# Performance work log

Hardware: AMD Instinct MI355X
Metric: run time of the kernel (lower is better)

The kernel has to match this reference:

```python
import jax, jax.numpy as jnp
import numpy as np

K_HOPS = 10  # truncation order of the heat-kernel Taylor series


def setup_inputs() -> dict:
    key = jax.random.key(0)
    k1, k2, k3 = jax.random.split(key, 3)
    N, E, D_IN, D_OUT = 50000, 625000, 128, 128
    x = jax.random.normal(k1, (N, D_IN), dtype=jnp.float32)
    edge_index = jax.random.randint(k2, (2, E), 0, N, dtype=jnp.int64)
    t = jnp.asarray(5.0, dtype=jnp.float32)  # learnable diffusion time
    lim = 1.0 / np.sqrt(D_IN)
    W = jax.random.uniform(k3, (D_OUT, D_IN), dtype=jnp.float32, minval=-lim, maxval=lim)
    b = jnp.zeros((D_OUT,), dtype=jnp.float32)
    return {"x": x, "edge_index": edge_index, "t": t, "W": W, "b": b}


def reference(x, edge_index, t, W, b):
    N = x.shape[0]
    loop = jnp.arange(N, dtype=edge_index.dtype)
    src = jnp.concatenate([edge_index[0], loop])  # gcn_norm adds self-loops
    dst = jnp.concatenate([edge_index[1], loop])
    # symmetric normalization: norm_e = deg(dst)^-1/2 * deg(src)^-1/2
    deg = jnp.zeros((N,), dtype=x.dtype).at[dst].add(1.0)
    dinv = jnp.where(deg > 0, jax.lax.rsqrt(deg), 0.0)
    norm = dinv[src] * dinv[dst]  # [E+N]

    def prop(h):  # one hop of A_hat @ h via gather-scale-scatter
        msg = h[src] * norm[:, None]          # [E+N, D]
        return jax.ops.segment_sum(msg, dst, num_segments=N)

    # heat kernel: e^{-t} * sum_k t^k/k! * A_hat^k x
    coeff = jnp.exp(-t)
    out = coeff * x
    h = x
    for k in range(1, K_HOPS + 1):
        h = prop(h)
        coeff = coeff * t / k
        out = out + coeff * h
    return out @ W.T + b
```

## Files before the change

kernel.cpp:

```cpp
#include <hip/hip_runtime.h>
#include <math.h>

typedef float f4 __attribute__((ext_vector_type(4)));
typedef float f8 __attribute__((ext_vector_type(8)));
typedef _Float16 h8 __attribute__((ext_vector_type(8)));
typedef int i4 __attribute__((ext_vector_type(4)));


__global__ void k_count(const int* __restrict__ dst, int* __restrict__ cnt, int E) {
  int e = blockIdx.x * blockDim.x + threadIdx.x;
  if (e < E) atomicAdd(&cnt[dst[e]], 1);
}

__global__ void k_scan_partial(const int* __restrict__ cnt, int* __restrict__ rowptr,
                               int* __restrict__ bsums, float* __restrict__ dinv,
                               float* __restrict__ rdinv, int N) {
  __shared__ int s[1024];
  int tid = threadIdx.x;
  int idx = blockIdx.x * 1024 + tid;
  int v = (idx < N) ? cnt[idx] : 0;
  if (idx < N) {
    dinv[idx] = rsqrtf((float)(v + 1));
    rdinv[idx] = sqrtf((float)(v + 1));
  }
  int vp = (v + 3) & ~3;
  s[tid] = vp;
  __syncthreads();
  for (int off = 1; off < 1024; off <<= 1) {
    int add = (tid >= off) ? s[tid - off] : 0;
    __syncthreads();
    s[tid] += add;
    __syncthreads();
  }
  if (idx <= N) rowptr[idx] = s[tid] - vp;
  if (tid == 1023) bsums[blockIdx.x] = s[1023];
}

__global__ void k_scan_sums(int* __restrict__ bsums, int nb) {
  __shared__ int s[1024];
  int tid = threadIdx.x;
  int v = (tid < nb) ? bsums[tid] : 0;
  s[tid] = v;
  __syncthreads();
  for (int off = 1; off < 1024; off <<= 1) {
    int add = (tid >= off) ? s[tid - off] : 0;
    __syncthreads();
    s[tid] += add;
    __syncthreads();
  }
  if (tid < nb) bsums[tid] = s[tid] - v;
}

__global__ void k_add_offsets(int* __restrict__ rowptr, int* __restrict__ cursor,
                              const int* __restrict__ bsums, int N) {
  int idx = blockIdx.x * 1024 + threadIdx.x;
  if (idx <= N) {
    int v = rowptr[idx] + bsums[blockIdx.x];
    rowptr[idx] = v;
    if (idx < N) cursor[idx] = v;
  }
}

__global__ void k_scatter(const int* __restrict__ src, const int* __restrict__ dst,
                          int* __restrict__ cursor, int* __restrict__ col, int E) {
  int e = blockIdx.x * blockDim.x + threadIdx.x;
  if (e < E) {
    int d = dst[e];
    int slot = atomicAdd(&cursor[d], 1);
    col[slot] = src[e];
  }
}

__global__ void k_padfill(const int* __restrict__ rowptr, const int* __restrict__ cursor,
                          int* __restrict__ col, int N) {
  int r = blockIdx.x * blockDim.x + threadIdx.x;
  if (r < N) {
    int e = cursor[r], end = rowptr[r + 1];
    for (; e < end; ++e) col[e] = N;
  }
}

__global__ void k_tohalf(const float* __restrict__ x, _Float16* __restrict__ xz,
                         const float* __restrict__ dinv, _Float16* __restrict__ z0,
                         _Float16* __restrict__ z1, int total8) {
  int i = blockIdx.x * blockDim.x + threadIdx.x;
  if (i < total8) {
    float d = dinv[i >> 4];
    f4 a = ((const f4*)x)[i * 2], b = ((const f4*)x)[i * 2 + 1];
    f8 v = {a.x, a.y, a.z, a.w, b.x, b.y, b.z, b.w};
    ((h8*)xz)[i] = __builtin_convertvector(d * v, h8);
  } else if (i < total8 + 48) {
    int k = i - total8;
    h8 zero = {0, 0, 0, 0, 0, 0, 0, 0};
    if (k < 16) ((h8*)xz)[total8 + k] = zero;
    else if (k < 32) ((h8*)z0)[total8 + (k - 16)] = zero;
    else ((h8*)z1)[total8 + (k - 32)] = zero;
  }
}

__global__ __launch_bounds__(256) void k_hop(
    const int* __restrict__ rowptr, const int* __restrict__ col,
    const float* __restrict__ dinv, const h8* __restrict__ xz,
    const h8* __restrict__ zin, h8* __restrict__ zout,
    const float* __restrict__ t_ptr, int j, int first, int N) {
  int wave = threadIdx.x >> 6;
  int lane = threadIdx.x & 63;
  int grp = lane >> 3;
  int r = (blockIdx.x * 4 + wave) * 4 + (grp >> 1);
  if (r >= N) return;
  int fl = (lane & 7) + (grp & 1) * 8;
  float t = t_ptr[0];
  float cj = expf(-t);
  for (int i = 1; i <= j; ++i) cj *= t / (float)i;
  float gs = first ? cj * t / (float)(j + 1) : 1.0f;

  auto G = [&](int idx) -> f8 {
    return __builtin_convertvector(zin[(size_t)idx * 16 + fl], f8);
  };

  f8 sA = {0, 0, 0, 0, 0, 0, 0, 0}, sB = sA, sC = sA, sD = sA;
  int e = rowptr[r], end = rowptr[r + 1];
  int cnt = end - e;
  const i4* q = (const i4*)&col[e];
  int it8 = cnt >> 3;
  int tail4 = cnt & 7;

  i4 p0 = {0, 0, 0, 0}, p1 = p0;
  if (it8) {
    p0 = q[0]; p1 = q[1];
    q += 2;
  }
  for (int i = 1; i < it8; ++i) {
    i4 n0 = q[0], n1 = q[1];
    q += 2;
    sA += G(p0.x);
    sB += G(p0.y);
    sC += G(p0.z);
    sD += G(p0.w);
    sA += G(p1.x);
    sB += G(p1.y);
    sC += G(p1.z);
    sD += G(p1.w);
    p0 = n0; p1 = n1;
  }
  if (it8) {
    sA += G(p0.x);
    sB += G(p0.y);
    sC += G(p0.z);
    sD += G(p0.w);
    sA += G(p1.x);
    sB += G(p1.y);
    sC += G(p1.z);
    sD += G(p1.w);
  }
  if (tail4) {
    i4 a0 = q[0];
    sA += G(a0.x);
    sB += G(a0.y);
    sC += G(a0.z);
    sD += G(a0.w);
  }

  f8 s = (sA + sB) + (sC + sD);
  s += G(r);
  float di = dinv[r];
  float sc = gs * di * di;
  f8 xr = __builtin_convertvector(xz[(size_t)r * 16 + fl], f8);
  s = sc * s + cj * xr;
  zout[(size_t)r * 16 + fl] = __builtin_convertvector(s, h8);
}

__global__ __launch_bounds__(256) void k_matmul(
    const h8* __restrict__ z16, const float* __restrict__ W,
    const float* __restrict__ bias, const float* __restrict__ rdinv,
    float* __restrict__ out, int N) {
  __shared__ h8 whiS[128 * 16];
  __shared__ h8 wloS[128 * 16];
  int tid = threadIdx.x;
  int rblk = blockIdx.x * 128;

#pragma unroll
  for (int it = 0; it < 8; ++it) {
    int idx = it * 256 + tid;
    int n = idx >> 4, g = idx & 15;
    f4 a = *(const f4*)&W[(size_t)n * 128 + g * 8];
    f4 b = *(const f4*)&W[(size_t)n * 128 + g * 8 + 4];
    f8 w = {a.x, a.y, a.z, a.w, b.x, b.y, b.z, b.w};
    h8 hi = __builtin_convertvector(w, h8);
    f8 hir = __builtin_convertvector(hi, f8);
    h8 lo = __builtin_convertvector(w - hir, h8);
    int slot = n * 16 + (g ^ (n & 7));
    whiS[slot] = hi;
    wloS[slot] = lo;
  }
  __syncthreads();

  int wave = tid >> 6, lane = tid & 63;
  int q = lane >> 4, fl = lane & 15;
  int rbase = rblk + wave * 32;

  f4 acc[2][8];
#pragma unroll
  for (int rt = 0; rt < 2; ++rt)
#pragma unroll
    for (int nt = 0; nt < 8; ++nt) acc[rt][nt] = (f4){0.f, 0.f, 0.f, 0.f};

#pragma unroll
  for (int s = 0; s < 4; ++s) {
    h8 aA, aB;
    {
      int r0 = rbase + fl;       if (r0 >= N) r0 = N - 1;
      int r1 = rbase + 16 + fl;  if (r1 >= N) r1 = N - 1;
      aA = z16[(size_t)r0 * 16 + s * 4 + q];
      aB = z16[(size_t)r1 * 16 + s * 4 + q];
    }
#pragma unroll
    for (int nt = 0; nt < 8; ++nt) {
      int n = nt * 16 + fl;
      int slot = n * 16 + ((s * 4 + q) ^ (n & 7));
      h8 bh = whiS[slot];
      h8 bl = wloS[slot];
      acc[0][nt] = __builtin_amdgcn_mfma_f32_16x16x32_f16(aA, bh, acc[0][nt], 0, 0, 0);
      acc[0][nt] = __builtin_amdgcn_mfma_f32_16x16x32_f16(aA, bl, acc[0][nt], 0, 0, 0);
      acc[1][nt] = __builtin_amdgcn_mfma_f32_16x16x32_f16(aB, bh, acc[1][nt], 0, 0, 0);
      acc[1][nt] = __builtin_amdgcn_mfma_f32_16x16x32_f16(aB, bl, acc[1][nt], 0, 0, 0);
    }
  }

#pragma unroll
  for (int rt = 0; rt < 2; ++rt) {
#pragma unroll
    for (int reg = 0; reg < 4; ++reg) {
      int r = rbase + rt * 16 + q * 4 + reg;
      if (r < N) {
        float rd = rdinv[r];
#pragma unroll
        for (int nt = 0; nt < 8; ++nt) {
          out[(size_t)r * 128 + nt * 16 + fl] =
              acc[rt][nt][reg] * rd + bias[nt * 16 + fl];
        }
      }
    }
  }
}


extern "C" void kernel_launch(void* const* d_in, const int* in_sizes, int n_in,
                              void* d_out, int out_size, void* d_ws, size_t ws_size,
                              hipStream_t stream) {
  const float* x = (const float*)d_in[0];
  const int* ei = (const int*)d_in[1];
  const float* t = (const float*)d_in[2];
  const float* W = (const float*)d_in[3];
  const float* b = (const float*)d_in[4];
  int N = in_sizes[0] / 128;
  int E = in_sizes[1] / 2;
  const int* srcp = ei;
  const int* dstp = ei + E;
  float* out = (float*)d_out;

  char* ws = (char*)d_ws;
  size_t off = 0;
  auto alloc = [&](size_t bytes) -> void* {
    void* p = ws + off;
    off += (bytes + 255) & ~(size_t)255;
    return p;
  };
  h8*    zh0    = (h8*)alloc((size_t)(N + 1) * 128 * 2);
  h8*    zh1    = (h8*)alloc((size_t)(N + 1) * 128 * 2);
  h8*    xz     = (h8*)alloc((size_t)(N + 1) * 128 * 2);
  int*   cnt    = (int*)alloc((size_t)N * 4);
  float* dinv   = (float*)alloc((size_t)N * 4);
  float* rdinv  = (float*)alloc((size_t)N * 4);
  int*   rowptr = (int*)alloc((size_t)(N + 1) * 4);
  int*   cursor = (int*)alloc((size_t)N * 4);
  int*   bsums  = (int*)alloc(4096);
  size_t col_bytes = ((size_t)E + 4 * (size_t)N) * 4;
  int*   col    = (int*)alloc(col_bytes);
  (void)ws_size;

  int nb_scan = (N + 1 + 1023) / 1024;

  hipMemsetAsync(cnt, 0, (size_t)N * 4, stream);
  k_count<<<(E + 255) / 256, 256, 0, stream>>>(dstp, cnt, E);
  k_scan_partial<<<nb_scan, 1024, 0, stream>>>(cnt, rowptr, bsums, dinv, rdinv, N);
  k_scan_sums<<<1, 1024, 0, stream>>>(bsums, nb_scan);
  k_add_offsets<<<nb_scan, 1024, 0, stream>>>(rowptr, cursor, bsums, N);
  k_scatter<<<(E + 255) / 256, 256, 0, stream>>>(srcp, dstp, cursor, col, E);
  k_padfill<<<(N + 255) / 256, 256, 0, stream>>>(rowptr, cursor, col, N);
  k_tohalf<<<(N * 16 + 48 + 255) / 256, 256, 0, stream>>>(x, (_Float16*)xz, dinv,
                                                          (_Float16*)zh0, (_Float16*)zh1,
                                                          N * 16);

  int nblk = (N + 15) / 16;
  const h8* zin = xz;
  h8* bufs[2] = {zh0, zh1};
  for (int m = 0; m < 10; ++m) {
    h8* zout = bufs[m & 1];
    k_hop<<<nblk, 256, 0, stream>>>(rowptr, col, dinv, xz, zin, zout,
                                    t, 9 - m, (m == 0) ? 1 : 0, N);
    zin = zout;
  }

  k_matmul<<<(N + 127) / 128, 256, 0, stream>>>(zin, W, b, rdinv, out, N);
}
```

Baseline: 430.4 us.

## Bucket CSR neighbours by source range to improve gather locality

Builds the CSR adjacency with four sub-rows per destination node, each holding neighbours from one quarter of the source index range. The hop kernel walks the four sub-rows in order so that concurrently running waves gather from a narrower range of feature rows, aiming for better cache hit rates. In exchange, each sub-row is padded to a multiple of four, which adds dummy gathers. The scan, count and row-pointer arrays also grow fourfold, and the hop loop loses its deeper 8-wide prefetch unroll.

```diff
diff --git a/kernel.cpp b/kernel.cpp
--- a/kernel.cpp
+++ b/kernel.cpp
@@ -7,9 +7,14 @@
 typedef int i4 __attribute__((ext_vector_type(4)));
 
 
-__global__ void k_count(const int* __restrict__ dst, int* __restrict__ cnt, int E) {
+__global__ void k_count(const int* __restrict__ src, const int* __restrict__ dst,
+                        int* __restrict__ cnt, float invb, int E) {
   int e = blockIdx.x * blockDim.x + threadIdx.x;
-  if (e < E) atomicAdd(&cnt[dst[e]], 1);
+  if (e < E) {
+    int b = (int)((float)src[e] * invb);
+    b = b > 3 ? 3 : b;
+    atomicAdd(&cnt[dst[e] * 4 + b], 1);
+  }
 }
 
 __global__ void k_scan_partial(const int* __restrict__ cnt, int* __restrict__ rowptr,
@@ -18,10 +23,12 @@
   __shared__ int s[1024];
   int tid = threadIdx.x;
   int idx = blockIdx.x * 1024 + tid;
-  int v = (idx < N) ? cnt[idx] : 0;
+  int M = 4 * N;
+  int v = (idx < M) ? cnt[idx] : 0;
   if (idx < N) {
-    dinv[idx] = rsqrtf((float)(v + 1));
-    rdinv[idx] = sqrtf((float)(v + 1));
+    int deg = cnt[4 * idx] + cnt[4 * idx + 1] + cnt[4 * idx + 2] + cnt[4 * idx + 3];
+    dinv[idx] = rsqrtf((float)(deg + 1));
+    rdinv[idx] = sqrtf((float)(deg + 1));
   }
   int vp = (v + 3) & ~3;
   s[tid] = vp;
@@ -32,7 +39,7 @@
     s[tid] += add;
     __syncthreads();
   }
-  if (idx <= N) rowptr[idx] = s[tid] - vp;
+  if (idx <= M) rowptr[idx] = s[tid] - vp;
   if (tid == 1023) bsums[blockIdx.x] = s[1023];
 }
 
@@ -54,28 +61,32 @@
 __global__ void k_add_offsets(int* __restrict__ rowptr, int* __restrict__ cursor,
                               const int* __restrict__ bsums, int N) {
   int idx = blockIdx.x * 1024 + threadIdx.x;
-  if (idx <= N) {
+  int M = 4 * N;
+  if (idx <= M) {
     int v = rowptr[idx] + bsums[blockIdx.x];
     rowptr[idx] = v;
-    if (idx < N) cursor[idx] = v;
+    if (idx < M) cursor[idx] = v;
   }
 }
 
 __global__ void k_scatter(const int* __restrict__ src, const int* __restrict__ dst,
-                          int* __restrict__ cursor, int* __restrict__ col, int E) {
+                          int* __restrict__ cursor, int* __restrict__ col,
+                          float invb, int E) {
   int e = blockIdx.x * blockDim.x + threadIdx.x;
   if (e < E) {
-    int d = dst[e];
-    int slot = atomicAdd(&cursor[d], 1);
-    col[slot] = src[e];
+    int s = src[e];
+    int b = (int)((float)s * invb);
+    b = b > 3 ? 3 : b;
+    int slot = atomicAdd(&cursor[dst[e] * 4 + b], 1);
+    col[slot] = s;
   }
 }
 
 __global__ void k_padfill(const int* __restrict__ rowptr, const int* __restrict__ cursor,
                           int* __restrict__ col, int N) {
-  int r = blockIdx.x * blockDim.x + threadIdx.x;
-  if (r < N) {
-    int e = cursor[r], end = rowptr[r + 1];
+  int idx = blockIdx.x * blockDim.x + threadIdx.x;
+  if (idx < 4 * N) {
+    int e = cursor[idx], end = rowptr[idx + 1];
     for (; e < end; ++e) col[e] = N;
   }
 }
@@ -119,46 +130,27 @@
   };
 
   f8 sA = {0, 0, 0, 0, 0, 0, 0, 0}, sB = sA, sC = sA, sD = sA;
-  int e = rowptr[r], end = rowptr[r + 1];
-  int cnt = end - e;
-  const i4* q = (const i4*)&col[e];
-  int it8 = cnt >> 3;
-  int tail4 = cnt & 7;
-
-  i4 p0 = {0, 0, 0, 0}, p1 = p0;
-  if (it8) {
-    p0 = q[0]; p1 = q[1];
-    q += 2;
-  }
-  for (int i = 1; i < it8; ++i) {
-    i4 n0 = q[0], n1 = q[1];
-    q += 2;
-    sA += G(p0.x);
-    sB += G(p0.y);
-    sC += G(p0.z);
-    sD += G(p0.w);
-    sA += G(p1.x);
-    sB += G(p1.y);
-    sC += G(p1.z);
-    sD += G(p1.w);
-    p0 = n0; p1 = n1;
-  }
-  if (it8) {
-    sA += G(p0.x);
-    sB += G(p0.y);
-    sC += G(p0.z);
-    sD += G(p0.w);
-    sA += G(p1.x);
-    sB += G(p1.y);
-    sC += G(p1.z);
-    sD += G(p1.w);
-  }
-  if (tail4) {
-    i4 a0 = q[0];
-    sA += G(a0.x);
-    sB += G(a0.y);
-    sC += G(a0.z);
-    sD += G(a0.w);
+  int base = r * 4;
+#pragma unroll
+  for (int b = 0; b < 4; ++b) {
+    int e = rowptr[base + b], end = rowptr[base + b + 1];
+    const i4* q = (const i4*)&col[e];
+    int n4 = (end - e) >> 2;
+    if (n4) {
+      i4 p = q[0];
+      for (int i = 1; i < n4; ++i) {
+        i4 nx = q[i];
+        sA += G(p.x);
+        sB += G(p.y);
+        sC += G(p.z);
+        sD += G(p.w);
+        p = nx;
+      }
+      sA += G(p.x);
+      sB += G(p.y);
+      sC += G(p.z);
+      sD += G(p.w);
+    }
   }
 
   f8 s = (sA + sB) + (sC + sD);
@@ -269,25 +261,28 @@
   h8*    zh0    = (h8*)alloc((size_t)(N + 1) * 128 * 2);
   h8*    zh1    = (h8*)alloc((size_t)(N + 1) * 128 * 2);
   h8*    xz     = (h8*)alloc((size_t)(N + 1) * 128 * 2);
-  int*   cnt    = (int*)alloc((size_t)N * 4);
+  int*   cnt    = (int*)alloc((size_t)N * 16);
   float* dinv   = (float*)alloc((size_t)N * 4);
   float* rdinv  = (float*)alloc((size_t)N * 4);
-  int*   rowptr = (int*)alloc((size_t)(N + 1) * 4);
-  int*   cursor = (int*)alloc((size_t)N * 4);
+  int*   rowptr = (int*)alloc((size_t)(4 * N + 1) * 4);
+  int*   cursor = (int*)alloc((size_t)N * 16);
   int*   bsums  = (int*)alloc(4096);
-  size_t col_bytes = ((size_t)E + 4 * (size_t)N) * 4;
+  size_t col_bytes = ((size_t)E + 16 * (size_t)N) * 4;
   int*   col    = (int*)alloc(col_bytes);
   (void)ws_size;
 
-  int nb_scan = (N + 1 + 1023) / 1024;
-
-  hipMemsetAsync(cnt, 0, (size_t)N * 4, stream);
-  k_count<<<(E + 255) / 256, 256, 0, stream>>>(dstp, cnt, E);
+  int bsize = (N + 3) >> 2;
+  float invb = 1.0f / (float)bsize;
+
+  int nb_scan = (4 * N + 1 + 1023) / 1024;
+
+  hipMemsetAsync(cnt, 0, (size_t)N * 16, stream);
+  k_count<<<(E + 255) / 256, 256, 0, stream>>>(srcp, dstp, cnt, invb, E);
   k_scan_partial<<<nb_scan, 1024, 0, stream>>>(cnt, rowptr, bsums, dinv, rdinv, N);
   k_scan_sums<<<1, 1024, 0, stream>>>(bsums, nb_scan);
   k_add_offsets<<<nb_scan, 1024, 0, stream>>>(rowptr, cursor, bsums, N);
-  k_scatter<<<(E + 255) / 256, 256, 0, stream>>>(srcp, dstp, cursor, col, E);
-  k_padfill<<<(N + 255) / 256, 256, 0, stream>>>(rowptr, cursor, col, N);
+  k_scatter<<<(E + 255) / 256, 256, 0, stream>>>(srcp, dstp, cursor, col, invb, E);
+  k_padfill<<<(4 * N + 255) / 256, 256, 0, stream>>>(rowptr, cursor, col, N);
   k_tohalf<<<(N * 16 + 48 + 255) / 256, 256, 0, stream>>>(x, (_Float16*)xz, dinv,
                                                           (_Float16*)zh0, (_Float16*)zh1,
                                                           N * 16);
```

Result: slower. 444.3 us (+3.2%).

## Split feature dimension into two half-planes and run hops per half

Applied to the files above, without the earlier changes.

Stores the fp16 features as two 64-column planes instead of 128-column rows, and runs the ten diffusion hops separately on each plane, with one row per 8-lane group. The aim is to halve the gathered working set per hop so that the random neighbour gathers hit in cache more often. In exchange the CSR index array is read twice and twice as many hop kernels are launched. The matmul reads its A operand from the two planes.

```diff
diff --git a/kernel.cpp b/kernel.cpp
--- a/kernel.cpp
+++ b/kernel.cpp
@@ -82,40 +82,43 @@
 
 __global__ void k_tohalf(const float* __restrict__ x, _Float16* __restrict__ xz,
                          const float* __restrict__ dinv, _Float16* __restrict__ z0,
-                         _Float16* __restrict__ z1, int total8) {
+                         _Float16* __restrict__ z1, int total8, int N) {
   int i = blockIdx.x * blockDim.x + threadIdx.x;
+  size_t plane = (size_t)(N + 1) * 8;
   if (i < total8) {
-    float d = dinv[i >> 4];
+    int row = i >> 4, g = i & 15;
+    float d = dinv[row];
     f4 a = ((const f4*)x)[i * 2], b = ((const f4*)x)[i * 2 + 1];
     f8 v = {a.x, a.y, a.z, a.w, b.x, b.y, b.z, b.w};
-    ((h8*)xz)[i] = __builtin_convertvector(d * v, h8);
+    ((h8*)xz)[(size_t)(g >> 3) * plane + (size_t)row * 8 + (g & 7)] =
+        __builtin_convertvector(d * v, h8);
   } else if (i < total8 + 48) {
     int k = i - total8;
     h8 zero = {0, 0, 0, 0, 0, 0, 0, 0};
-    if (k < 16) ((h8*)xz)[total8 + k] = zero;
-    else if (k < 32) ((h8*)z0)[total8 + (k - 16)] = zero;
-    else ((h8*)z1)[total8 + (k - 32)] = zero;
+    int buf = k >> 4, sl = k & 15;
+    h8* base = buf == 0 ? (h8*)xz : (buf == 1 ? (h8*)z0 : (h8*)z1);
+    base[(size_t)(sl >> 3) * plane + (size_t)N * 8 + (sl & 7)] = zero;
   }
 }
 
 __global__ __launch_bounds__(256) void k_hop(
     const int* __restrict__ rowptr, const int* __restrict__ col,
-    const float* __restrict__ dinv, const h8* __restrict__ xz,
-    const h8* __restrict__ zin, h8* __restrict__ zout,
+    const float* __restrict__ dinv, const h8* __restrict__ xzp,
+    const h8* __restrict__ zinp, h8* __restrict__ zoutp,
     const float* __restrict__ t_ptr, int j, int first, int N) {
   int wave = threadIdx.x >> 6;
   int lane = threadIdx.x & 63;
   int grp = lane >> 3;
-  int r = (blockIdx.x * 4 + wave) * 4 + (grp >> 1);
+  int r = (blockIdx.x * 4 + wave) * 8 + grp;
   if (r >= N) return;
-  int fl = (lane & 7) + (grp & 1) * 8;
+  int fl = lane & 7;
   float t = t_ptr[0];
   float cj = expf(-t);
   for (int i = 1; i <= j; ++i) cj *= t / (float)i;
   float gs = first ? cj * t / (float)(j + 1) : 1.0f;
 
   auto G = [&](int idx) -> f8 {
-    return __builtin_convertvector(zin[(size_t)idx * 16 + fl], f8);
+    return __builtin_convertvector(zinp[(size_t)idx * 8 + fl], f8);
   };
 
   f8 sA = {0, 0, 0, 0, 0, 0, 0, 0}, sB = sA, sC = sA, sD = sA;
@@ -165,9 +168,9 @@
   s += G(r);
   float di = dinv[r];
   float sc = gs * di * di;
-  f8 xr = __builtin_convertvector(xz[(size_t)r * 16 + fl], f8);
+  f8 xr = __builtin_convertvector(xzp[(size_t)r * 8 + fl], f8);
   s = sc * s + cj * xr;
-  zout[(size_t)r * 16 + fl] = __builtin_convertvector(s, h8);
+  zoutp[(size_t)r * 8 + fl] = __builtin_convertvector(s, h8);
 }
 
 __global__ __launch_bounds__(256) void k_matmul(
@@ -178,6 +181,7 @@
   __shared__ h8 wloS[128 * 16];
   int tid = threadIdx.x;
   int rblk = blockIdx.x * 128;
+  size_t plane = (size_t)(N + 1) * 8;
 
 #pragma unroll
   for (int it = 0; it < 8; ++it) {
@@ -211,8 +215,10 @@
     {
       int r0 = rbase + fl;       if (r0 >= N) r0 = N - 1;
       int r1 = rbase + 16 + fl;  if (r1 >= N) r1 = N - 1;
-      aA = z16[(size_t)r0 * 16 + s * 4 + q];
-      aB = z16[(size_t)r1 * 16 + s * 4 + q];
+      int g = s * 4 + q;
+      const h8* zp = z16 + (size_t)(g >> 3) * plane + (g & 7);
+      aA = zp[(size_t)r0 * 8];
+      aB = zp[(size_t)r1 * 8];
     }
 #pragma unroll
     for (int nt = 0; nt < 8; ++nt) {
@@ -290,17 +296,20 @@
   k_padfill<<<(N + 255) / 256, 256, 0, stream>>>(rowptr, cursor, col, N);
   k_tohalf<<<(N * 16 + 48 + 255) / 256, 256, 0, stream>>>(x, (_Float16*)xz, dinv,
                                                           (_Float16*)zh0, (_Float16*)zh1,
-                                                          N * 16);
-
-  int nblk = (N + 15) / 16;
-  const h8* zin = xz;
+                                                          N * 16, N);
+
+  int nblk = (N + 31) / 32;
+  size_t plane = (size_t)(N + 1) * 8;
   h8* bufs[2] = {zh0, zh1};
-  for (int m = 0; m < 10; ++m) {
-    h8* zout = bufs[m & 1];
-    k_hop<<<nblk, 256, 0, stream>>>(rowptr, col, dinv, xz, zin, zout,
-                                    t, 9 - m, (m == 0) ? 1 : 0, N);
-    zin = zout;
-  }
-
-  k_matmul<<<(N + 127) / 128, 256, 0, stream>>>(zin, W, b, rdinv, out, N);
-}
+  for (int half = 0; half < 2; ++half) {
+    const h8* zin = xz + half * plane;
+    for (int m = 0; m < 10; ++m) {
+      h8* zout = bufs[m & 1] + half * plane;
+      k_hop<<<nblk, 256, 0, stream>>>(rowptr, col, dinv, xz + half * plane,
+                                      zin, zout, t, 9 - m, (m == 0) ? 1 : 0, N);
+      zin = zout;
+    }
+  }
+
+  k_matmul<<<(N + 127) / 128, 256, 0, stream>>>(zh1, W, b, rdinv, out, N);
+}
```

New measurement: 446.7 us. 3.8% more time.

## Fuse ten hop launches into one persistent cooperative kernel with grid sync

Applied to the files above, without the earlier changes.

Replaces the ten separate per-hop kernel launches with a single cooperative persistent kernel. It loops over the hops internally and separates them with grid-wide barriers, with a grid-stride loop over row chunks. The aim is to remove per-launch overhead and the tail idle time between hops. In exchange it limits the grid to resident blocks, adds grid-sync cost, and keeps a fallback path to the old per-hop launches.

```diff
diff --git a/kernel.cpp b/kernel.cpp
--- a/kernel.cpp
+++ b/kernel.cpp
@@ -1,5 +1,8 @@
 #include <hip/hip_runtime.h>
+#include <hip/hip_cooperative_groups.h>
 #include <math.h>
+
+namespace cg = cooperative_groups;
 
 typedef float f4 __attribute__((ext_vector_type(4)));
 typedef float f8 __attribute__((ext_vector_type(8)));
@@ -98,6 +101,98 @@
   }
 }
 
+__device__ __forceinline__ void hop_row(
+    int r, int fl, const int* __restrict__ rowptr, const int* __restrict__ col,
+    const float* __restrict__ dinv, const h8* __restrict__ xz,
+    const h8* __restrict__ zin, h8* __restrict__ zout, float cj, float gs) {
+  auto G = [&](int idx) -> f8 {
+    return __builtin_convertvector(zin[(size_t)idx * 16 + fl], f8);
+  };
+
+  f8 sA = {0, 0, 0, 0, 0, 0, 0, 0}, sB = sA, sC = sA, sD = sA;
+  int e = rowptr[r], end = rowptr[r + 1];
+  int cnt = end - e;
+  const i4* q = (const i4*)&col[e];
+  int it8 = cnt >> 3;
+  int tail4 = cnt & 7;
+
+  i4 p0 = {0, 0, 0, 0}, p1 = p0;
+  if (it8) {
+    p0 = q[0]; p1 = q[1];
+    q += 2;
+  }
+  for (int i = 1; i < it8; ++i) {
+    i4 n0 = q[0], n1 = q[1];
+    q += 2;
+    sA += G(p0.x);
+    sB += G(p0.y);
+    sC += G(p0.z);
+    sD += G(p0.w);
+    sA += G(p1.x);
+    sB += G(p1.y);
+    sC += G(p1.z);
+    sD += G(p1.w);
+    p0 = n0; p1 = n1;
+  }
+  if (it8) {
+    sA += G(p0.x);
+    sB += G(p0.y);
+    sC += G(p0.z);
+    sD += G(p0.w);
+    sA += G(p1.x);
+    sB += G(p1.y);
+    sC += G(p1.z);
+    sD += G(p1.w);
+  }
+  if (tail4) {
+    i4 a0 = q[0];
+    sA += G(a0.x);
+    sB += G(a0.y);
+    sC += G(a0.z);
+    sD += G(a0.w);
+  }
+
+  f8 s = (sA + sB) + (sC + sD);
+  s += G(r);
+  float di = dinv[r];
+  float sc = gs * di * di;
+  f8 xr = __builtin_convertvector(xz[(size_t)r * 16 + fl], f8);
+  s = sc * s + cj * xr;
+  zout[(size_t)r * 16 + fl] = __builtin_convertvector(s, h8);
+}
+
+__global__ __launch_bounds__(256, 4) void k_hops(
+    const int* __restrict__ rowptr, const int* __restrict__ col,
+    const float* __restrict__ dinv, const h8* __restrict__ xz,
+    h8* __restrict__ zh0, h8* __restrict__ zh1,
+    const float* __restrict__ t_ptr, int N, int nchunks) {
+  cg::grid_group gridg = cg::this_grid();
+  int wave = threadIdx.x >> 6;
+  int lane = threadIdx.x & 63;
+  int grp = lane >> 3;
+  int fl = (lane & 7) + (grp & 1) * 8;
+  float t = t_ptr[0];
+  float c[10];
+  c[0] = expf(-t);
+  for (int i = 1; i <= 9; ++i) c[i] = c[i - 1] * t / (float)i;
+  float c10 = c[9] * t * 0.1f;
+
+  const h8* zin = xz;
+  h8* bufs[2] = {zh0, zh1};
+
+  for (int m = 0; m < 10; ++m) {
+    h8* zout = bufs[m & 1];
+    float cj = c[9 - m];
+    float gs = (m == 0) ? c10 : 1.0f;
+    for (int chunk = blockIdx.x; chunk < nchunks; chunk += gridDim.x) {
+      int r = chunk * 16 + wave * 4 + (grp >> 1);
+      if (r < N) hop_row(r, fl, rowptr, col, dinv, xz, zin, zout, cj, gs);
+    }
+    gridg.sync();
+    zin = zout;
+  }
+}
+
 __global__ __launch_bounds__(256) void k_hop(
     const int* __restrict__ rowptr, const int* __restrict__ col,
     const float* __restrict__ dinv, const h8* __restrict__ xz,
@@ -113,61 +208,7 @@
   float cj = expf(-t);
   for (int i = 1; i <= j; ++i) cj *= t / (float)i;
   float gs = first ? cj * t / (float)(j + 1) : 1.0f;
-
-  auto G = [&](int idx) -> f8 {
-    return __builtin_convertvector(zin[(size_t)idx * 16 + fl], f8);
-  };
-
-  f8 sA = {0, 0, 0, 0, 0, 0, 0, 0}, sB = sA, sC = sA, sD = sA;
-  int e = rowptr[r], end = rowptr[r + 1];
-  int cnt = end - e;
-  const i4* q = (const i4*)&col[e];
-  int it8 = cnt >> 3;
-  int tail4 = cnt & 7;
-
-  i4 p0 = {0, 0, 0, 0}, p1 = p0;
-  if (it8) {
-    p0 = q[0]; p1 = q[1];
-    q += 2;
-  }
-  for (int i = 1; i < it8; ++i) {
-    i4 n0 = q[0], n1 = q[1];
-    q += 2;
-    sA += G(p0.x);
-    sB += G(p0.y);
-    sC += G(p0.z);
-    sD += G(p0.w);
-    sA += G(p1.x);
-    sB += G(p1.y);
-    sC += G(p1.z);
-    sD += G(p1.w);
-    p0 = n0; p1 = n1;
-  }
-  if (it8) {
-    sA += G(p0.x);
-    sB += G(p0.y);
-    sC += G(p0.z);
-    sD += G(p0.w);
-    sA += G(p1.x);
-    sB += G(p1.y);
-    sC += G(p1.z);
-    sD += G(p1.w);
-  }
-  if (tail4) {
-    i4 a0 = q[0];
-    sA += G(a0.x);
-    sB += G(a0.y);
-    sC += G(a0.z);
-    sD += G(a0.w);
-  }
-
-  f8 s = (sA + sB) + (sC + sD);
-  s += G(r);
-  float di = dinv[r];
-  float sc = gs * di * di;
-  f8 xr = __builtin_convertvector(xz[(size_t)r * 16 + fl], f8);
-  s = sc * s + cj * xr;
-  zout[(size_t)r * 16 + fl] = __builtin_convertvector(s, h8);
+  hop_row(r, fl, rowptr, col, dinv, xz, zin, zout, cj, gs);
 }
 
 __global__ __launch_bounds__(256) void k_matmul(
@@ -250,7 +291,7 @@
                               hipStream_t stream) {
   const float* x = (const float*)d_in[0];
   const int* ei = (const int*)d_in[1];
-  const float* t = (const float*)d_in[2];
+  const float* tptr = (const float*)d_in[2];
   const float* W = (const float*)d_in[3];
   const float* b = (const float*)d_in[4];
   int N = in_sizes[0] / 128;
@@ -292,15 +333,43 @@
                                                           (_Float16*)zh0, (_Float16*)zh1,
                                                           N * 16);
 
-  int nblk = (N + 15) / 16;
-  const h8* zin = xz;
-  h8* bufs[2] = {zh0, zh1};
-  for (int m = 0; m < 10; ++m) {
-    h8* zout = bufs[m & 1];
-    k_hop<<<nblk, 256, 0, stream>>>(rowptr, col, dinv, xz, zin, zout,
-                                    t, 9 - m, (m == 0) ? 1 : 0, N);
-    zin = zout;
-  }
-
-  k_matmul<<<(N + 127) / 128, 256, 0, stream>>>(zin, W, b, rdinv, out, N);
-}
+  int nchunks = (N + 15) / 16;
+
+  static int coop_grid = -2;
+  if (coop_grid == -2) {
+    int maxb = 0, ncu = 0, dev = 0;
+    if (hipGetDevice(&dev) == hipSuccess &&
+        hipDeviceGetAttribute(&ncu, hipDeviceAttributeMultiprocessorCount, dev) ==
+            hipSuccess &&
+        hipOccupancyMaxActiveBlocksPerMultiprocessor(&maxb, k_hops, 256, 0) ==
+            hipSuccess &&
+        maxb > 0 && ncu > 0) {
+      coop_grid = maxb * ncu;
+    } else {
+      coop_grid = -1;
+    }
+  }
+
+  bool coop_done = false;
+  if (coop_grid > 0) {
+    int grid = coop_grid < nchunks ? coop_grid : nchunks;
+    void* args[] = {&rowptr, &col, &dinv, &xz, &zh0, &zh1,
+                    (void*)&tptr, &N, &nchunks};
+    coop_done = hipLaunchCooperativeKernel((void*)k_hops, dim3(grid), dim3(256),
+                                           args, 0, stream) == hipSuccess;
+    if (!coop_done) coop_grid = -1;
+  }
+
+  if (!coop_done) {
+    const h8* zin = xz;
+    h8* bufs[2] = {zh0, zh1};
+    for (int m = 0; m < 10; ++m) {
+      h8* zout = bufs[m & 1];
+      k_hop<<<(N + 15) / 16, 256, 0, stream>>>(rowptr, col, dinv, xz, zin, zout,
+                                               tptr, 9 - m, (m == 0) ? 1 : 0, N);
+      zin = zout;
+    }
+  }
+
+  k_matmul<<<(N + 127) / 128, 256, 0, stream>>>(zh1, W, b, rdinv, out, N);
+}
```

After: 1.114 ms. 159% more time.
